# Optimization experiments

Measured on AMD Instinct MI355X. Metric: run time of the kernel, lower is better.

Reference implementation:

```python
import jax, jax.numpy as jnp
import numpy as np

N_NODES = 100000
N_EDGES = 1600000
NUM_GRAPHS = 128
IN_F = 32
K = 3  # TAGConv default number of hops


def setup_inputs() -> dict:
    key = jax.random.key(0)
    ks = jax.random.split(key, 12)
    x = jax.random.normal(ks[0], (N_NODES, IN_F), dtype=jnp.float32)
    edge_index = jax.random.randint(ks[1], (2, N_EDGES), 0, N_NODES, dtype=jnp.int32)
    batch = jnp.sort(jax.random.randint(ks[2], (N_NODES,), 0, NUM_GRAPHS, dtype=jnp.int32))
    edge_weight = jax.random.uniform(ks[3], (N_EDGES,), dtype=jnp.float32)
    # TAGConv params: K+1 weight matrices per layer (bias shared per layer)
    s1 = 1.0 / np.sqrt(IN_F)
    s2 = 1.0 / np.sqrt(8)
    s3 = 1.0 / np.sqrt(32)
    W1 = jax.random.uniform(ks[4], (K + 1, IN_F, 8), jnp.float32, -s1, s1)
    b1 = jax.random.uniform(ks[5], (8,), jnp.float32, -s1, s1)
    W2 = jax.random.uniform(ks[6], (K + 1, 8, 16), jnp.float32, -s2, s2)
    b2 = jax.random.uniform(ks[7], (16,), jnp.float32, -s2, s2)
    Wfc = jax.random.uniform(ks[8], (32, 2), jnp.float32, -s3, s3)
    bfc = jax.random.uniform(ks[9], (2,), jnp.float32, -s3, s3)
    return {"x": x, "edge_index": edge_index, "batch": batch, "edge_weight": edge_weight,
            "W1": W1, "b1": b1, "W2": W2, "b2": b2, "Wfc": Wfc, "bfc": bfc}


def reference(x, edge_index, batch, edge_weight, W1, b1, W2, b2, Wfc, bfc):
    src, dst = edge_index[0], edge_index[1]
    n = x.shape[0]
    # gcn_norm without self-loops (TAGConv default): D^-1/2 A D^-1/2
    deg = jax.ops.segment_sum(edge_weight, dst, num_segments=n)
    dinv = jnp.where(deg > 0, jax.lax.rsqrt(jnp.maximum(deg, 1e-30)), 0.0)
    norm = dinv[src] * edge_weight * dinv[dst]

    def tag_conv(h, W, b):
        out = h @ W[0]
        for k in range(1, W.shape[0]):
            # sparse propagate: gather at src, scale, scatter-add at dst
            h = jax.ops.segment_sum(h[src] * norm[:, None], dst, num_segments=n)
            out = out + h @ W[k]
        return out + b

    h = jax.nn.relu(tag_conv(x, W1, b1))
    h = jax.nn.relu(tag_conv(h, W2, b2))
    # global max pool + global mean pool over graphs in the batch
    mx = jax.ops.segment_max(h, batch, num_segments=NUM_GRAPHS)
    cnt = jax.ops.segment_sum(jnp.ones((n,), h.dtype), batch, num_segments=NUM_GRAPHS)
    mean = jax.ops.segment_sum(h, batch, num_segments=NUM_GRAPHS) / jnp.maximum(cnt, 1.0)[:, None]
    return jnp.concatenate([mx, mean], axis=1) @ Wfc + bfc
```

## Files before the change

### kernel.cpp

```cpp
#include <hip/hip_runtime.h>

constexpr int NN = 100000;
constexpr int NE = 1600000;
constexpr int NG = 128;

constexpr int SCAN_T = 256;
constexpr int SCAN_B = (NN + SCAN_T - 1) / SCAN_T;

struct __align__(8) Ent { int s; float nw; };


__global__ void k_rank(const int* __restrict__ dst, int* __restrict__ cnt,
                       int* __restrict__ rank, int ne) {
    int e = blockIdx.x * blockDim.x + threadIdx.x;
    if (e < ne) rank[e] = atomicAdd(&cnt[dst[e]], 1);
}


__global__ void k_scan1(const int* __restrict__ cnt, int* __restrict__ bsum, int nn) {
    __shared__ int s[SCAN_T];
    int i = blockIdx.x * SCAN_T + threadIdx.x;
    s[threadIdx.x] = (i < nn) ? cnt[i] : 0;
    __syncthreads();
    for (int off = SCAN_T / 2; off > 0; off >>= 1) {
        if (threadIdx.x < off) s[threadIdx.x] += s[threadIdx.x + off];
        __syncthreads();
    }
    if (threadIdx.x == 0) bsum[blockIdx.x] = s[0];
}

__global__ void k_scan2(int* __restrict__ bsum, int nb) {
    __shared__ int s[512];
    int t = threadIdx.x;
    s[t] = (t < nb) ? bsum[t] : 0;
    __syncthreads();
    for (int off = 1; off < 512; off <<= 1) {
        int v = (t >= off) ? s[t - off] : 0;
        __syncthreads();
        s[t] += v;
        __syncthreads();
    }
    if (t < nb) bsum[t] = (t > 0) ? s[t - 1] : 0;
}

__global__ void k_scan3(const int* __restrict__ cnt, const int* __restrict__ bsum,
                        int* __restrict__ row_ptr, int nn) {
    __shared__ int s[SCAN_T];
    int t = threadIdx.x;
    int i = blockIdx.x * SCAN_T + t;
    int v = (i < nn) ? cnt[i] : 0;
    s[t] = v;
    __syncthreads();
    for (int off = 1; off < SCAN_T; off <<= 1) {
        int u = (t >= off) ? s[t - off] : 0;
        __syncthreads();
        s[t] += u;
        __syncthreads();
    }
    int incl = s[t];
    int base = bsum[blockIdx.x];
    if (i < nn) {
        row_ptr[i] = base + incl - v;
        if (i == nn - 1) row_ptr[nn] = base + incl;
    }
}

__global__ void k_scatter2(const int* __restrict__ src, const int* __restrict__ dst,
                           const float* __restrict__ w, const int* __restrict__ row_ptr,
                           const int* __restrict__ rank, Ent* __restrict__ csr, int ne) {
    int e = blockIdx.x * blockDim.x + threadIdx.x;
    if (e >= ne) return;
    int slot = row_ptr[dst[e]] + rank[e];
    Ent en; en.s = src[e]; en.nw = w[e];
    csr[slot] = en;
}

__global__ void k_degi(const int* __restrict__ row_ptr, const Ent* __restrict__ csr,
                       float* __restrict__ dinv, int nn) {
    int tid = blockIdx.x * blockDim.x + threadIdx.x;
    int n = tid >> 3, lane = tid & 7;
    if (n >= nn) return;
    int beg = row_ptr[n], end = row_ptr[n + 1];
    float s = 0.f;
    for (int e = beg + lane; e < end; e += 8) s += csr[e].nw;
    s += __shfl_xor(s, 1, 64);
    s += __shfl_xor(s, 2, 64);
    s += __shfl_xor(s, 4, 64);
    if (lane == 0) dinv[n] = s > 0.f ? rsqrtf(fmaxf(s, 1e-30f)) : 0.f;
}

__global__ void k_norm2(const int* __restrict__ row_ptr, Ent* __restrict__ csr,
                        const float* __restrict__ dinv, int nn) {
    int tid = blockIdx.x * blockDim.x + threadIdx.x;
    int n = tid >> 3, lane = tid & 7;
    if (n >= nn) return;
    int beg = row_ptr[n], end = row_ptr[n + 1];
    float dn = dinv[n];
    for (int e = beg + lane; e < end; e += 8) {
        Ent en = csr[e];
        csr[e].nw = dinv[en.s] * en.nw * dn;
    }
}

template <int FIN, int FOUT>
__global__ void k_mm4(const float* __restrict__ h, const float* __restrict__ W,
                      float* __restrict__ t, int nn) {
    __shared__ float sW[4 * FIN * FOUT];
    for (int i = threadIdx.x; i < 4 * FIN * FOUT; i += blockDim.x) sW[i] = W[i];
    __syncthreads();
    int n = blockIdx.x * blockDim.x + threadIdx.x;
    if (n >= nn) return;
    float hr[FIN];
    const float4* hp = reinterpret_cast<const float4*>(h + (size_t)n * FIN);
#pragma unroll
    for (int f = 0; f < FIN / 4; ++f) {
        float4 v = hp[f];
        hr[4 * f + 0] = v.x; hr[4 * f + 1] = v.y;
        hr[4 * f + 2] = v.z; hr[4 * f + 3] = v.w;
    }
#pragma unroll
    for (int k = 0; k < 4; ++k) {
        float acc[FOUT];
#pragma unroll
        for (int j = 0; j < FOUT; ++j) acc[j] = 0.f;
#pragma unroll
        for (int i = 0; i < FIN; ++i) {
            float hv = hr[i];
            const float* wrow = &sW[(k * FIN + i) * FOUT];
#pragma unroll
            for (int j = 0; j < FOUT; ++j) acc[j] = fmaf(hv, wrow[j], acc[j]);
        }
        float4* op = reinterpret_cast<float4*>(t + ((size_t)k * nn + n) * FOUT);
#pragma unroll
        for (int j4 = 0; j4 < FOUT / 4; ++j4)
            op[j4] = make_float4(acc[4 * j4], acc[4 * j4 + 1], acc[4 * j4 + 2], acc[4 * j4 + 3]);
    }
}

template <int F, bool EPI>
__global__ void k_pull(const int* __restrict__ row_ptr, const Ent* __restrict__ csr,
                       const float* __restrict__ hin, const float* __restrict__ add,
                       const float* __restrict__ b, float* __restrict__ hout, int nn) {
    int g = blockIdx.x * (blockDim.x / F) + threadIdx.x / F;
    int lane = threadIdx.x & (F - 1);
    if (g >= nn) return;
    int beg = row_ptr[g], end = row_ptr[g + 1];
    float acc0 = 0.f, acc1 = 0.f;
    int e = beg;
    for (; e + 1 < end; e += 2) {
        Ent e0 = csr[e], e1 = csr[e + 1];
        acc0 = fmaf(hin[(size_t)e0.s * F + lane], e0.nw, acc0);
        acc1 = fmaf(hin[(size_t)e1.s * F + lane], e1.nw, acc1);
    }
    if (e < end) {
        Ent e0 = csr[e];
        acc0 = fmaf(hin[(size_t)e0.s * F + lane], e0.nw, acc0);
    }
    float r = acc0 + acc1 + add[(size_t)g * F + lane];
    if (EPI) r = fmaxf(r + b[lane], 0.f);
    hout[(size_t)g * F + lane] = r;
}


__global__ void k_bounds(const int* __restrict__ batch, int* __restrict__ start, int nn) {
    int i = blockIdx.x * blockDim.x + threadIdx.x;
    if (i >= nn) return;
    int b = batch[i];
    int prev = (i == 0) ? -1 : batch[i - 1];
    for (int g = prev + 1; g <= b; ++g) start[g] = i;
    if (i == nn - 1) {
        for (int g = b + 1; g <= NG; ++g) start[g] = nn;
    }
}

__global__ void k_pool2(const float* __restrict__ h, const int* __restrict__ start,
                        const float* __restrict__ Wfc, const float* __restrict__ bfc,
                        float* __restrict__ out) {
    int g = blockIdx.x;
    int beg = start[g], end = start[g + 1];
    int tid = threadIdx.x;
    int feat = tid & 15, grp = tid >> 4;
    float mx = 0.f, sm = 0.f;
    for (int n = beg + grp; n < end; n += 16) {
        float v = h[(size_t)n * 16 + feat];
        mx = fmaxf(mx, v);
        sm += v;
    }
    mx = fmaxf(mx, __shfl_xor(mx, 16, 64));
    sm += __shfl_xor(sm, 16, 64);
    mx = fmaxf(mx, __shfl_xor(mx, 32, 64));
    sm += __shfl_xor(sm, 32, 64);
    __shared__ float smx[4][16], ssm[4][16];
    int wave = tid >> 6;
    int lane = tid & 63;
    if (lane < 16) { smx[wave][feat] = mx; ssm[wave][feat] = sm; }
    __syncthreads();
    if (tid < 16) {
        float m = fmaxf(fmaxf(smx[0][tid], smx[1][tid]), fmaxf(smx[2][tid], smx[3][tid]));
        float s = ssm[0][tid] + ssm[1][tid] + ssm[2][tid] + ssm[3][tid];
        smx[0][tid] = m;
        ssm[0][tid] = (end > beg) ? s / (float)(end - beg) : 0.f;
    }
    __syncthreads();
    if (tid < 2) {
        float acc = bfc[tid];
#pragma unroll
        for (int i = 0; i < 16; ++i) acc += smx[0][i] * Wfc[i * 2 + tid];
#pragma unroll
        for (int i = 0; i < 16; ++i) acc += ssm[0][i] * Wfc[(16 + i) * 2 + tid];
        out[g * 2 + tid] = acc;
    }
}


extern "C" void kernel_launch(void* const* d_in, const int* in_sizes, int n_in,
                              void* d_out, int out_size, void* d_ws, size_t ws_size,
                              hipStream_t stream) {
    const float* x    = (const float*)d_in[0];
    const int*   eidx = (const int*)d_in[1];
    const int*   srcp = eidx;
    const int*   dstp = eidx + NE;
    const int*   batch= (const int*)d_in[2];
    const float* ew   = (const float*)d_in[3];
    const float* W1   = (const float*)d_in[4];
    const float* b1   = (const float*)d_in[5];
    const float* W2   = (const float*)d_in[6];
    const float* b2   = (const float*)d_in[7];
    const float* Wfc  = (const float*)d_in[8];
    const float* bfc  = (const float*)d_in[9];
    float* out = (float*)d_out;

    constexpr size_t NN8  = (size_t)NN * 8;
    constexpr size_t NN16 = (size_t)NN * 16;

    float* dinv     = (float*)d_ws;
    int*   cnt      = (int*)(dinv + NN);
    int*   row_ptr  = cnt + NN;
    int*   rank     = row_ptr + NN + 4;
    Ent*   csr      = (Ent*)(rank + NE);
    float* uni      = (float*)(csr + NE);
    float* h1       = uni + 5 * NN16;
    int*   gstart   = (int*)(h1 + NN8);
    int*   bsum     = gstart + NG + 4;

    float* T  = uni;
    float* P  = uni + 2 * NN16;
    float* P2 = P + NN8;
    float* U    = uni;
    float* q    = uni + 4 * NN16;
    float* q2   = U + 3 * NN16;
    float* out2 = U + 2 * NN16;

    const int BLK = 256;
    const int gE = (NE + BLK - 1) / BLK;
    const int gN = (NN + BLK - 1) / BLK;
    const int gP8  = (NN + (BLK / 8) - 1) / (BLK / 8);
    const int gP16 = (NN + (BLK / 16) - 1) / (BLK / 16);
    const int gN8  = (NN * 8 + BLK - 1) / BLK;

    hipMemsetAsync(cnt, 0, (size_t)NN * sizeof(int), stream);
    k_rank<<<gE, BLK, 0, stream>>>(dstp, cnt, rank, NE);
    k_scan1<<<SCAN_B, SCAN_T, 0, stream>>>(cnt, bsum, NN);
    k_scan2<<<1, 512, 0, stream>>>(bsum, SCAN_B);
    k_scan3<<<SCAN_B, SCAN_T, 0, stream>>>(cnt, bsum, row_ptr, NN);
    k_scatter2<<<gE, BLK, 0, stream>>>(srcp, dstp, ew, row_ptr, rank, csr, NE);
    k_degi<<<gN8, BLK, 0, stream>>>(row_ptr, csr, dinv, NN);
    k_norm2<<<gN8, BLK, 0, stream>>>(row_ptr, csr, dinv, NN);
    k_bounds<<<gN, BLK, 0, stream>>>(batch, gstart, NN);

    k_mm4<32, 8><<<gN, BLK, 0, stream>>>(x, W1, T, NN);
    k_pull<8, false><<<gP8, BLK, 0, stream>>>(row_ptr, csr, T + 3 * NN8, T + 2 * NN8, nullptr, P, NN);
    k_pull<8, false><<<gP8, BLK, 0, stream>>>(row_ptr, csr, P, T + 1 * NN8, nullptr, P2, NN);
    k_pull<8, true ><<<gP8, BLK, 0, stream>>>(row_ptr, csr, P2, T, b1, h1, NN);

    k_mm4<8, 16><<<gN, BLK, 0, stream>>>(h1, W2, U, NN);
    k_pull<16, false><<<gP16, BLK, 0, stream>>>(row_ptr, csr, U + 3 * NN16, U + 2 * NN16, nullptr, q, NN);
    k_pull<16, false><<<gP16, BLK, 0, stream>>>(row_ptr, csr, q, U + 1 * NN16, nullptr, q2, NN);
    k_pull<16, true ><<<gP16, BLK, 0, stream>>>(row_ptr, csr, q2, U, b2, out2, NN);

    k_pool2<<<NG, 256, 0, stream>>>(out2, gstart, Wfc, bfc, out);
}
```

Before: 362.2 us.

## Factor symmetric normalization into node scaling and pad CSR rows for float4 loads

Drops the per-edge normalization pass. Edge weights stay raw, and the D^-1/2 factors are applied per node: the last projection in the matmul kernel and each pull kernel's output are scaled by dinv. CSR rows are padded to even length with zero entries, so the pull and degree kernels can read two edges per float4 load with four accumulators. Rank is stored as ushort and the rank/scatter kernels process four edges per thread with vector loads. The risks are a bigger CSR buffer, a ushort rank that overflows if a node's in-degree exceeds 65535, and a slightly different rounding order.

```diff
diff --git a/kernel.cpp b/kernel.cpp
--- a/kernel.cpp
+++ b/kernel.cpp
@@ -10,17 +10,24 @@
 struct __align__(8) Ent { int s; float nw; };
 
 
-__global__ void k_rank(const int* __restrict__ dst, int* __restrict__ cnt,
-                       int* __restrict__ rank, int ne) {
-    int e = blockIdx.x * blockDim.x + threadIdx.x;
-    if (e < ne) rank[e] = atomicAdd(&cnt[dst[e]], 1);
+__global__ void k_rank(const int4* __restrict__ dst4, int* __restrict__ cnt,
+                       ushort4* __restrict__ rank4, int ne4) {
+    int i = blockIdx.x * blockDim.x + threadIdx.x;
+    if (i >= ne4) return;
+    int4 d = dst4[i];
+    ushort4 r;
+    r.x = (ushort)atomicAdd(&cnt[d.x], 1);
+    r.y = (ushort)atomicAdd(&cnt[d.y], 1);
+    r.z = (ushort)atomicAdd(&cnt[d.z], 1);
+    r.w = (ushort)atomicAdd(&cnt[d.w], 1);
+    rank4[i] = r;
 }
 
 
 __global__ void k_scan1(const int* __restrict__ cnt, int* __restrict__ bsum, int nn) {
     __shared__ int s[SCAN_T];
     int i = blockIdx.x * SCAN_T + threadIdx.x;
-    s[threadIdx.x] = (i < nn) ? cnt[i] : 0;
+    s[threadIdx.x] = (i < nn) ? ((cnt[i] + 1) & ~1) : 0;
     __syncthreads();
     for (int off = SCAN_T / 2; off > 0; off >>= 1) {
         if (threadIdx.x < off) s[threadIdx.x] += s[threadIdx.x + off];
@@ -48,7 +55,7 @@
     __shared__ int s[SCAN_T];
     int t = threadIdx.x;
     int i = blockIdx.x * SCAN_T + t;
-    int v = (i < nn) ? cnt[i] : 0;
+    int v = (i < nn) ? ((cnt[i] + 1) & ~1) : 0;
     s[t] = v;
     __syncthreads();
     for (int off = 1; off < SCAN_T; off <<= 1) {
@@ -65,46 +72,47 @@
     }
 }
 
-__global__ void k_scatter2(const int* __restrict__ src, const int* __restrict__ dst,
-                           const float* __restrict__ w, const int* __restrict__ row_ptr,
-                           const int* __restrict__ rank, Ent* __restrict__ csr, int ne) {
-    int e = blockIdx.x * blockDim.x + threadIdx.x;
-    if (e >= ne) return;
-    int slot = row_ptr[dst[e]] + rank[e];
-    Ent en; en.s = src[e]; en.nw = w[e];
-    csr[slot] = en;
-}
-
-__global__ void k_degi(const int* __restrict__ row_ptr, const Ent* __restrict__ csr,
+__global__ void k_scatter2(const int4* __restrict__ src4, const int4* __restrict__ dst4,
+                           const float4* __restrict__ w4, const int* __restrict__ row_ptr,
+                           const ushort4* __restrict__ rank4, Ent* __restrict__ csr, int ne4) {
+    int i = blockIdx.x * blockDim.x + threadIdx.x;
+    if (i >= ne4) return;
+    int4 s = src4[i]; int4 d = dst4[i]; float4 w = w4[i]; ushort4 r = rank4[i];
+    Ent e0; e0.s = s.x; e0.nw = w.x; csr[row_ptr[d.x] + r.x] = e0;
+    Ent e1; e1.s = s.y; e1.nw = w.y; csr[row_ptr[d.y] + r.y] = e1;
+    Ent e2; e2.s = s.z; e2.nw = w.z; csr[row_ptr[d.z] + r.z] = e2;
+    Ent e3; e3.s = s.w; e3.nw = w.w; csr[row_ptr[d.w] + r.w] = e3;
+}
+
+__global__ void k_pad(const int* __restrict__ cnt, const int* __restrict__ row_ptr,
+                      Ent* __restrict__ csr, int nn) {
+    int n = blockIdx.x * blockDim.x + threadIdx.x;
+    if (n < nn && (cnt[n] & 1)) {
+        Ent z; z.s = 0; z.nw = 0.f;
+        csr[row_ptr[n] + cnt[n]] = z;
+    }
+}
+
+__global__ void k_degi(const int* __restrict__ row_ptr, const float4* __restrict__ csr4,
                        float* __restrict__ dinv, int nn) {
     int tid = blockIdx.x * blockDim.x + threadIdx.x;
     int n = tid >> 3, lane = tid & 7;
     if (n >= nn) return;
-    int beg = row_ptr[n], end = row_ptr[n + 1];
+    int beg = row_ptr[n] >> 1, end = row_ptr[n + 1] >> 1;
     float s = 0.f;
-    for (int e = beg + lane; e < end; e += 8) s += csr[e].nw;
+    for (int p = beg + lane; p < end; p += 8) {
+        float4 a = csr4[p];
+        s += a.y + a.w;
+    }
     s += __shfl_xor(s, 1, 64);
     s += __shfl_xor(s, 2, 64);
     s += __shfl_xor(s, 4, 64);
     if (lane == 0) dinv[n] = s > 0.f ? rsqrtf(fmaxf(s, 1e-30f)) : 0.f;
 }
 
-__global__ void k_norm2(const int* __restrict__ row_ptr, Ent* __restrict__ csr,
-                        const float* __restrict__ dinv, int nn) {
-    int tid = blockIdx.x * blockDim.x + threadIdx.x;
-    int n = tid >> 3, lane = tid & 7;
-    if (n >= nn) return;
-    int beg = row_ptr[n], end = row_ptr[n + 1];
-    float dn = dinv[n];
-    for (int e = beg + lane; e < end; e += 8) {
-        Ent en = csr[e];
-        csr[e].nw = dinv[en.s] * en.nw * dn;
-    }
-}
-
 template <int FIN, int FOUT>
 __global__ void k_mm4(const float* __restrict__ h, const float* __restrict__ W,
-                      float* __restrict__ t, int nn) {
+                      const float* __restrict__ dinv, float* __restrict__ t, int nn) {
     __shared__ float sW[4 * FIN * FOUT];
     for (int i = threadIdx.x; i < 4 * FIN * FOUT; i += blockDim.x) sW[i] = W[i];
     __syncthreads();
@@ -118,6 +126,7 @@
         hr[4 * f + 0] = v.x; hr[4 * f + 1] = v.y;
         hr[4 * f + 2] = v.z; hr[4 * f + 3] = v.w;
     }
+    float dv = dinv[n];
 #pragma unroll
     for (int k = 0; k < 4; ++k) {
         float acc[FOUT];
@@ -130,6 +139,10 @@
 #pragma unroll
             for (int j = 0; j < FOUT; ++j) acc[j] = fmaf(hv, wrow[j], acc[j]);
         }
+        if (k == 3) {
+#pragma unroll
+            for (int j = 0; j < FOUT; ++j) acc[j] *= dv;
+        }
         float4* op = reinterpret_cast<float4*>(t + ((size_t)k * nn + n) * FOUT);
 #pragma unroll
         for (int j4 = 0; j4 < FOUT / 4; ++j4)
@@ -137,27 +150,33 @@
     }
 }
 
-template <int F, bool EPI>
-__global__ void k_pull(const int* __restrict__ row_ptr, const Ent* __restrict__ csr,
+template <int F, bool FINAL>
+__global__ void k_pull(const int* __restrict__ row_ptr, const float4* __restrict__ csr4,
+                       const float* __restrict__ dinv,
                        const float* __restrict__ hin, const float* __restrict__ add,
                        const float* __restrict__ b, float* __restrict__ hout, int nn) {
     int g = blockIdx.x * (blockDim.x / F) + threadIdx.x / F;
     int lane = threadIdx.x & (F - 1);
     if (g >= nn) return;
-    int beg = row_ptr[g], end = row_ptr[g + 1];
-    float acc0 = 0.f, acc1 = 0.f;
-    int e = beg;
-    for (; e + 1 < end; e += 2) {
-        Ent e0 = csr[e], e1 = csr[e + 1];
-        acc0 = fmaf(hin[(size_t)e0.s * F + lane], e0.nw, acc0);
-        acc1 = fmaf(hin[(size_t)e1.s * F + lane], e1.nw, acc1);
-    }
-    if (e < end) {
-        Ent e0 = csr[e];
-        acc0 = fmaf(hin[(size_t)e0.s * F + lane], e0.nw, acc0);
-    }
-    float r = acc0 + acc1 + add[(size_t)g * F + lane];
-    if (EPI) r = fmaxf(r + b[lane], 0.f);
+    int p = row_ptr[g] >> 1, end = row_ptr[g + 1] >> 1;
+    float acc0 = 0.f, acc1 = 0.f, acc2 = 0.f, acc3 = 0.f;
+    for (; p + 2 <= end; p += 2) {
+        float4 a = csr4[p], c = csr4[p + 1];
+        acc0 = fmaf(hin[(size_t)__float_as_int(a.x) * F + lane], a.y, acc0);
+        acc1 = fmaf(hin[(size_t)__float_as_int(a.z) * F + lane], a.w, acc1);
+        acc2 = fmaf(hin[(size_t)__float_as_int(c.x) * F + lane], c.y, acc2);
+        acc3 = fmaf(hin[(size_t)__float_as_int(c.z) * F + lane], c.w, acc3);
+    }
+    if (p < end) {
+        float4 a = csr4[p];
+        acc0 = fmaf(hin[(size_t)__float_as_int(a.x) * F + lane], a.y, acc0);
+        acc1 = fmaf(hin[(size_t)__float_as_int(a.z) * F + lane], a.w, acc1);
+    }
+    float acc = (acc0 + acc1) + (acc2 + acc3);
+    float dv = dinv[g];
+    float r;
+    if (FINAL) r = fmaxf(dv * acc + add[(size_t)g * F + lane] + b[lane], 0.f);
+    else       r = dv * (dv * acc + add[(size_t)g * F + lane]);
     hout[(size_t)g * F + lane] = r;
 }
 
@@ -233,15 +252,15 @@
     constexpr size_t NN8  = (size_t)NN * 8;
     constexpr size_t NN16 = (size_t)NN * 16;
 
-    float* dinv     = (float*)d_ws;
-    int*   cnt      = (int*)(dinv + NN);
-    int*   row_ptr  = cnt + NN;
-    int*   rank     = row_ptr + NN + 4;
-    Ent*   csr      = (Ent*)(rank + NE);
-    float* uni      = (float*)(csr + NE);
-    float* h1       = uni + 5 * NN16;
-    int*   gstart   = (int*)(h1 + NN8);
-    int*   bsum     = gstart + NG + 4;
+    float*  dinv    = (float*)d_ws;
+    int*    cnt     = (int*)(dinv + NN);
+    int*    row_ptr = cnt + NN;
+    ushort* rank    = (ushort*)(row_ptr + NN + 4);
+    Ent*    csr     = (Ent*)((int*)(void*)rank + NE / 2);
+    float*  uni     = (float*)(csr + NE + NN);
+    float*  h1      = uni + 5 * NN16;
+    int*    gstart  = (int*)(h1 + NN8);
+    int*    bsum    = gstart + NG + 4;
 
     float* T  = uni;
     float* P  = uni + 2 * NN16;
@@ -251,32 +270,37 @@
     float* q2   = U + 3 * NN16;
     float* out2 = U + 2 * NN16;
 
+    const float4* csr4 = (const float4*)csr;
+
     const int BLK = 256;
-    const int gE = (NE + BLK - 1) / BLK;
-    const int gN = (NN + BLK - 1) / BLK;
+    const int NE4 = NE / 4;
+    const int gE4 = (NE4 + BLK - 1) / BLK;
+    const int gN  = (NN + BLK - 1) / BLK;
     const int gP8  = (NN + (BLK / 8) - 1) / (BLK / 8);
     const int gP16 = (NN + (BLK / 16) - 1) / (BLK / 16);
     const int gN8  = (NN * 8 + BLK - 1) / BLK;
 
     hipMemsetAsync(cnt, 0, (size_t)NN * sizeof(int), stream);
-    k_rank<<<gE, BLK, 0, stream>>>(dstp, cnt, rank, NE);
+    k_rank<<<gE4, BLK, 0, stream>>>((const int4*)dstp, cnt, (ushort4*)rank, NE4);
     k_scan1<<<SCAN_B, SCAN_T, 0, stream>>>(cnt, bsum, NN);
     k_scan2<<<1, 512, 0, stream>>>(bsum, SCAN_B);
     k_scan3<<<SCAN_B, SCAN_T, 0, stream>>>(cnt, bsum, row_ptr, NN);
-    k_scatter2<<<gE, BLK, 0, stream>>>(srcp, dstp, ew, row_ptr, rank, csr, NE);
-    k_degi<<<gN8, BLK, 0, stream>>>(row_ptr, csr, dinv, NN);
-    k_norm2<<<gN8, BLK, 0, stream>>>(row_ptr, csr, dinv, NN);
+    k_scatter2<<<gE4, BLK, 0, stream>>>((const int4*)srcp, (const int4*)dstp,
+                                        (const float4*)ew, row_ptr, (const ushort4*)rank,
+                                        csr, NE4);
+    k_pad<<<gN, BLK, 0, stream>>>(cnt, row_ptr, csr, NN);
+    k_degi<<<gN8, BLK, 0, stream>>>(row_ptr, csr4, dinv, NN);
     k_bounds<<<gN, BLK, 0, stream>>>(batch, gstart, NN);
 
-    k_mm4<32, 8><<<gN, BLK, 0, stream>>>(x, W1, T, NN);
-    k_pull<8, false><<<gP8, BLK, 0, stream>>>(row_ptr, csr, T + 3 * NN8, T + 2 * NN8, nullptr, P, NN);
-    k_pull<8, false><<<gP8, BLK, 0, stream>>>(row_ptr, csr, P, T + 1 * NN8, nullptr, P2, NN);
-    k_pull<8, true ><<<gP8, BLK, 0, stream>>>(row_ptr, csr, P2, T, b1, h1, NN);
-
-    k_mm4<8, 16><<<gN, BLK, 0, stream>>>(h1, W2, U, NN);
-    k_pull<16, false><<<gP16, BLK, 0, stream>>>(row_ptr, csr, U + 3 * NN16, U + 2 * NN16, nullptr, q, NN);
-    k_pull<16, false><<<gP16, BLK, 0, stream>>>(row_ptr, csr, q, U + 1 * NN16, nullptr, q2, NN);
-    k_pull<16, true ><<<gP16, BLK, 0, stream>>>(row_ptr, csr, q2, U, b2, out2, NN);
+    k_mm4<32, 8><<<gN, BLK, 0, stream>>>(x, W1, dinv, T, NN);
+    k_pull<8, false><<<gP8, BLK, 0, stream>>>(row_ptr, csr4, dinv, T + 3 * NN8, T + 2 * NN8, nullptr, P, NN);
+    k_pull<8, false><<<gP8, BLK, 0, stream>>>(row_ptr, csr4, dinv, P, T + 1 * NN8, nullptr, P2, NN);
+    k_pull<8, true ><<<gP8, BLK, 0, stream>>>(row_ptr, csr4, dinv, P2, T, b1, h1, NN);
+
+    k_mm4<8, 16><<<gN, BLK, 0, stream>>>(h1, W2, dinv, U, NN);
+    k_pull<16, false><<<gP16, BLK, 0, stream>>>(row_ptr, csr4, dinv, U + 3 * NN16, U + 2 * NN16, nullptr, q, NN);
+    k_pull<16, false><<<gP16, BLK, 0, stream>>>(row_ptr, csr4, dinv, q, U + 1 * NN16, nullptr, q2, NN);
+    k_pull<16, true ><<<gP16, BLK, 0, stream>>>(row_ptr, csr4, dinv, q2, U, b2, out2, NN);
 
     k_pool2<<<NG, 256, 0, stream>>>(out2, gstart, Wfc, bfc, out);
 }
```

Result: faster. 309.8 us (-14.5%).
